# Kernel optimization log

Measured on AMD Instinct MI355X. Metric: run time of the kernel, lower is better.

## Reference

```python
import jax, jax.numpy as jnp
import numpy as np

B, N, DIM, H, DH = 8, 1024, 768, 12, 64  # batch, seq, d_model, heads, dim_head
INNER = H * DH


def setup_inputs() -> dict:
    key = jax.random.key(0)
    ks = jax.random.split(key, 6)
    s = 1.0 / np.sqrt(DIM)
    return {
        "x": jax.random.normal(ks[0], (B, N, DIM), dtype=jnp.float32),
        "Wq": jax.random.normal(ks[1], (DIM, INNER), dtype=jnp.float32) * s,
        "Wkv": jax.random.normal(ks[2], (DIM, 2 * INNER), dtype=jnp.float32) * s,
        "mix_pre": jax.random.normal(ks[3], (H, H), dtype=jnp.float32) * (1.0 / H),
        "mix_post": jax.random.normal(ks[4], (H, H), dtype=jnp.float32) * (1.0 / H),
        "Wo": jax.random.normal(ks[5], (INNER, DIM), dtype=jnp.float32) * s,
        "bo": jnp.zeros((DIM,), dtype=jnp.float32),
    }


def reference(x, Wq, Wkv, mix_pre, mix_post, Wo, bo):
    scale = DH ** -0.5
    q = x @ Wq                                   # [B,N,INNER]
    kv = x @ Wkv                                 # [B,N,2*INNER]
    k, v = jnp.split(kv, 2, axis=-1)
    split_heads = lambda t: t.reshape(B, N, H, DH).transpose(0, 2, 1, 3)  # [B,H,N,DH]
    q, k, v = split_heads(q), split_heads(k), split_heads(v)
    dots = jnp.einsum('bhid,bhjd->bhij', q, k) * scale
    dots = jnp.einsum('bhij,hg->bgij', dots, mix_pre)      # talking-heads pre-softmax
    attn = jax.nn.softmax(dots, axis=-1)
    attn = jnp.einsum('bhij,hg->bgij', attn, mix_post)     # talking-heads post-softmax
    o = jnp.einsum('bhij,bhjd->bhid', attn, v)             # [B,H,N,DH]
    o = o.transpose(0, 2, 1, 3).reshape(B, N, INNER)
    return o @ Wo + bo
```

## Files before the change

### kernel.cpp

```cpp
#include <hip/hip_runtime.h>
#include <cstdint>
#include <cstddef>

typedef unsigned short u16;
typedef unsigned int u32;

typedef __bf16 bf16x8 __attribute__((ext_vector_type(8)));
typedef float f32x4 __attribute__((ext_vector_type(4)));
typedef u32 u32x4 __attribute__((ext_vector_type(4)));
typedef u32 u32x2 __attribute__((ext_vector_type(2)));

#if defined(__has_builtin)
#if __has_builtin(__builtin_amdgcn_global_load_lds)
#define USE_GLL 1
#endif
#endif

typedef const __attribute__((address_space(1))) u32 gas_u32;
typedef __attribute__((address_space(3))) u32 las_u32;

__device__ inline float bf2f(u16 u) {
    union { u32 i; float f; } c; c.i = ((u32)u) << 16; return c.f;
}
__device__ inline u16 f2bf(float f) {
    union { float f; u32 i; } c; c.f = f;
    u32 u = c.i;
    return (u16)((u + 0x7fffu + ((u >> 16) & 1u)) >> 16);
}
__device__ inline f32x4 mfma16(u32x4 a, u32x4 b, f32x4 c) {
    return __builtin_amdgcn_mfma_f32_16x16x32_bf16(
        __builtin_bit_cast(bf16x8, a), __builtin_bit_cast(bf16x8, b), c, 0, 0, 0);
}
__device__ inline u32x4 cvt8(const float* p) {
    f32x4 a = *(const f32x4*)p, b = *(const f32x4*)(p + 4);
    u32x4 v;
    v[0] = (u32)f2bf(a[0]) | ((u32)f2bf(a[1]) << 16);
    v[1] = (u32)f2bf(a[2]) | ((u32)f2bf(a[3]) << 16);
    v[2] = (u32)f2bf(b[0]) | ((u32)f2bf(b[1]) << 16);
    v[3] = (u32)f2bf(b[2]) | ((u32)f2bf(b[3]) << 16);
    return v;
}

__device__ inline void bar_lds() {
    asm volatile("s_waitcnt lgkmcnt(0)" ::: "memory");
    __builtin_amdgcn_s_barrier();
    __builtin_amdgcn_sched_barrier(0);
}

__global__ __launch_bounds__(64) void k_detect(const u16* __restrict__ x, u32* __restrict__ flag)
{
    const int lane = threadIdx.x;
    int cnt = 0;
#pragma unroll
    for (int i = 0; i < 4; i++) {
        u32 e = (x[lane * 4 + i] >> 7) & 0xFF;
        cnt += (e >= 115 && e <= 133) ? 1 : 0;
    }
#pragma unroll
    for (int off = 1; off < 64; off <<= 1) cnt += __shfl_xor(cnt, off);
    if (lane == 0) *flag = (cnt >= 192) ? 1u : 0u;
}

__global__ __launch_bounds__(256) void k_convert_x(
    const void* __restrict__ X, u16* __restrict__ xb, const u32* __restrict__ flag)
{
    const bool isb = (*flag != 0);
    const size_t i = ((size_t)blockIdx.x * 256 + threadIdx.x) * 8;
    if (isb) *(u32x4*)(xb + i) = *(const u32x4*)((const u16*)X + i);
    else     *(u32x4*)(xb + i) = cvt8((const float*)X + i);
}

__global__ __launch_bounds__(256) void k_transpose_w(
    const void* __restrict__ Wq, const void* __restrict__ Wkv, const void* __restrict__ Wo,
    u16* __restrict__ WT, u16* __restrict__ WoT, const u32* __restrict__ flag)
{
    const bool isb = (*flag != 0);
    __shared__ __align__(16) u16 t[64][72];
    const int z = blockIdx.z;
    const void* src; u16* dst; int C;
    if (z == 0)      { src = Wq;  dst = WT;             C = 768;  }
    else if (z == 1) { src = Wkv; dst = WT + 768 * 768; C = 1536; }
    else             { src = Wo;  dst = WoT;            C = 768;  }
    const int c0 = blockIdx.y * 64;
    if (c0 >= C) return;
    const int k0 = blockIdx.x * 64;
    const int tid = threadIdx.x;
    const int r = tid >> 3, cc = (tid & 7) * 8;
    if (isb) {
        const u16* s = (const u16*)src;
        for (int rr = r; rr < 64; rr += 32)
            *(u32x4*)&t[rr][cc] = *(const u32x4*)(s + (size_t)(k0 + rr) * C + c0 + cc);
    } else {
        const float* s = (const float*)src;
        for (int rr = r; rr < 64; rr += 32)
            *(u32x4*)&t[rr][cc] = cvt8(s + (size_t)(k0 + rr) * C + c0 + cc);
    }
    __syncthreads();
    const int kk = (tid & 7) * 8;
    for (int ccc = tid >> 3; ccc < 64; ccc += 32) {
        __align__(16) u16 tmp[8];
#pragma unroll
        for (int s = 0; s < 8; s++) tmp[s] = t[kk + s][ccc];
        *(u32x4*)(dst + (size_t)(c0 + ccc) * 768 + k0 + kk) = *(u32x4*)tmp;
    }
}

__global__ __launch_bounds__(256) void k_transpose_v(
    const u16* __restrict__ v, u16* __restrict__ vt)
{
    __shared__ __align__(16) u16 t[64][72];
    const int bh = blockIdx.z;
    const int t0 = blockIdx.x * 64;
    const int tid = threadIdx.x;
    const int r = tid >> 3, cc = (tid & 7) * 8;
    for (int rr = r; rr < 64; rr += 32)
        *(u32x4*)&t[rr][cc] = *(const u32x4*)(v + ((size_t)bh * 1024 + t0 + rr) * 64 + cc);
    __syncthreads();
    const int kk = (tid & 7) * 8;
    for (int ccc = tid >> 3; ccc < 64; ccc += 32) {
        __align__(16) u16 tmp[8];
#pragma unroll
        for (int s = 0; s < 8; s++) tmp[s] = t[kk + s][ccc];
        *(u32x4*)(vt + ((size_t)bh * 64 + ccc) * 1024 + t0 + kk) = *(u32x4*)tmp;
    }
}

__device__ inline void stage_tile(const u16* __restrict__ gA, const u16* __restrict__ gB,
                                  u16* As, u16* Bs, int w, int lane)
{
    const int sr = lane >> 2, sc = (lane & 3) * 8;
#pragma unroll
    for (int i = 0; i < 2; i++) {
        const int rA = w * 16 + i * 64;
        const u16* ga = gA + (size_t)(rA + sr) * 768 + sc;
        const u16* gb = gB + (size_t)(rA + sr) * 768 + sc;
#ifdef USE_GLL
        __builtin_amdgcn_global_load_lds((gas_u32*)ga, (las_u32*)&As[rA * 32], 16, 0, 0);
        __builtin_amdgcn_global_load_lds((gas_u32*)gb, (las_u32*)&Bs[rA * 32], 16, 0, 0);
#else
        *(u32x4*)&As[(rA + sr) * 32 + sc] = *(const u32x4*)ga;
        *(u32x4*)&Bs[(rA + sr) * 32 + sc] = *(const u32x4*)gb;
#endif
    }
}

__global__ __launch_bounds__(256) void k_gemm_qkv(
    const u16* __restrict__ Xb, const u16* __restrict__ WT,
    u16* __restrict__ qb, u16* __restrict__ kb, u16* __restrict__ vb)
{
    __shared__ __align__(16) u16 As[128 * 32];
    __shared__ __align__(16) u16 Bs[128 * 32];
    const int tid = threadIdx.x;
    const int w = tid >> 6, lane = tid & 63, quad = lane >> 4, l15 = lane & 15;
    const int wr = w >> 1, wc = w & 1;
    const int m0 = blockIdx.y * 128, c0 = blockIdx.x * 128;
    f32x4 acc[4][4];
#pragma unroll
    for (int i = 0; i < 4; i++)
#pragma unroll
        for (int j = 0; j < 4; j++) acc[i][j] = (f32x4){0.f, 0.f, 0.f, 0.f};

    for (int k0 = 0; k0 < 768; k0 += 32) {
        __syncthreads();
        stage_tile(Xb + (size_t)m0 * 768 + k0, WT + (size_t)c0 * 768 + k0, As, Bs, w, lane);
        __syncthreads();
        u32x4 af[4], bfv[4];
#pragma unroll
        for (int mi = 0; mi < 4; mi++)
            af[mi] = *(const u32x4*)&As[(wr * 64 + mi * 16 + l15) * 32 + quad * 8];
#pragma unroll
        for (int ni = 0; ni < 4; ni++)
            bfv[ni] = *(const u32x4*)&Bs[(wc * 64 + ni * 16 + l15) * 32 + quad * 8];
#pragma unroll
        for (int mi = 0; mi < 4; mi++)
#pragma unroll
            for (int ni = 0; ni < 4; ni++)
                acc[mi][ni] = mfma16(af[mi], bfv[ni], acc[mi][ni]);
    }
#pragma unroll
    for (int mi = 0; mi < 4; mi++)
#pragma unroll
        for (int ni = 0; ni < 4; ni++) {
            const int c = c0 + wc * 64 + ni * 16 + l15;
            const int sector = c / 768, hc = c % 768;
            const int h = hc >> 6, d = hc & 63;
            u16* dst = sector == 0 ? qb : (sector == 1 ? kb : vb);
#pragma unroll
            for (int r = 0; r < 4; r++) {
                const int tok = m0 + wr * 64 + mi * 16 + quad * 4 + r;
                const int b = tok >> 10, n = tok & 1023;
                dst[(((size_t)b * 12 + h) * 1024 + n) * 64 + d] = f2bf(acc[mi][ni][r]);
            }
        }
}

__global__ __launch_bounds__(256) void k_gemm_out(
    const u16* __restrict__ O, const u16* __restrict__ WoT, const void* __restrict__ bo,
    float* __restrict__ out, const u32* __restrict__ flag)
{
    const bool isb = (*flag != 0);
    __shared__ __align__(16) u16 As[128 * 32];
    __shared__ __align__(16) u16 Bs[128 * 32];
    const int tid = threadIdx.x;
    const int w = tid >> 6, lane = tid & 63, quad = lane >> 4, l15 = lane & 15;
    const int wr = w >> 1, wc = w & 1;
    const int m0 = blockIdx.y * 128, c0 = blockIdx.x * 128;
    f32x4 acc[4][4];
#pragma unroll
    for (int i = 0; i < 4; i++)
#pragma unroll
        for (int j = 0; j < 4; j++) acc[i][j] = (f32x4){0.f, 0.f, 0.f, 0.f};

    for (int k0 = 0; k0 < 768; k0 += 32) {
        __syncthreads();
        stage_tile(O + (size_t)m0 * 768 + k0, WoT + (size_t)c0 * 768 + k0, As, Bs, w, lane);
        __syncthreads();
        u32x4 af[4], bfv[4];
#pragma unroll
        for (int mi = 0; mi < 4; mi++)
            af[mi] = *(const u32x4*)&As[(wr * 64 + mi * 16 + l15) * 32 + quad * 8];
#pragma unroll
        for (int ni = 0; ni < 4; ni++)
            bfv[ni] = *(const u32x4*)&Bs[(wc * 64 + ni * 16 + l15) * 32 + quad * 8];
#pragma unroll
        for (int mi = 0; mi < 4; mi++)
#pragma unroll
            for (int ni = 0; ni < 4; ni++)
                acc[mi][ni] = mfma16(af[mi], bfv[ni], acc[mi][ni]);
    }
#pragma unroll
    for (int mi = 0; mi < 4; mi++)
#pragma unroll
        for (int ni = 0; ni < 4; ni++) {
            const int c = c0 + wc * 64 + ni * 16 + l15;
            const float biasv = isb ? bf2f(((const u16*)bo)[c]) : ((const float*)bo)[c];
#pragma unroll
            for (int r = 0; r < 4; r++) {
                const int tok = m0 + wr * 64 + mi * 16 + quad * 4 + r;
                out[(size_t)tok * 768 + c] = acc[mi][ni][r] + biasv;
            }
        }
}

__device__ inline void stage_e(const u16* __restrict__ src, u16* dst, int w, int lane)
{
#pragma unroll
    for (int c = 0; c < 2; c++) {
        const int off = ((w * 2 + c) * 64 + lane) * 8;
#ifdef USE_GLL
        __builtin_amdgcn_global_load_lds((gas_u32*)(src + off), (las_u32*)(dst + off), 16, 0, 0);
#else
        *(u32x4*)(dst + off) = *(const u32x4*)(src + off);
#endif
    }
}

__global__ __launch_bounds__(768) void k_attn(
    const u16* __restrict__ qb, const u16* __restrict__ kb, const u16* __restrict__ vt,
    const void* __restrict__ mixpre, const void* __restrict__ mixpost,
    u16* __restrict__ ob, u16* __restrict__ E, const u32* __restrict__ flag, int tiles)
{
    __shared__ __align__(16) u16 LDSU[18432];
    __shared__ float invlT[256];
    __shared__ __align__(16) u16 Eslab[2][12296];
    u16* SP   = LDSU;
    u32* SP32 = (u32*)LDSU;
    u16* Abuf = LDSU;
    float* red = (float*)LDSU;

    const bool isb = (*flag != 0);
    const int tid = threadIdx.x;
    const int w = tid >> 6, lane = tid & 63, quad = lane >> 4, l15 = lane & 15;
    const int bid = blockIdx.x;
    const int b = bid & 7;
    const int nq = gridDim.x >> 3;
    u16* Ewg = E + (size_t)bid * (16384 * 12);

    u32x4 apre = (u32x4){0, 0, 0, 0};
    float mpostF[8];
#pragma unroll
    for (int j = 0; j < 8; j++) {
        const int h = quad * 8 + j;
        mpostF[j] = 0.f;
        if (quad < 2 && l15 < 12 && h < 12) {
            mpostF[j] = isb ? bf2f(((const u16*)mixpost)[h * 12 + l15])
                            : ((const float*)mixpost)[h * 12 + l15];
            u16 v1 = isb ? ((const u16*)mixpre)[h * 12 + l15]
                         : f2bf(((const float*)mixpre)[h * 12 + l15]);
            apre[j >> 1] |= ((u32)v1) << ((j & 1) * 16);
        }
    }

    const u16* kh = kb + ((size_t)b * 12 + w) * 1024 * 64;
    const u16* vh = vt + ((size_t)b * 12 + w) * 64 * 1024;

    for (int tt = 0; tt < tiles; tt++) {
        const int qx = (bid >> 3) + tt * nq;
        const int i0 = qx * 16;

        for (int n = tid; n < 1024; n += 768) { SP32[n * 9 + 6] = 0; SP32[n * 9 + 7] = 0; }

        const u16* qh = qb + (((size_t)b * 12 + w) * 1024 + i0) * 64;
        u32x4 aq[2];
#pragma unroll
        for (int kc = 0; kc < 2; kc++)
            aq[kc] = *(const u32x4*)(qh + l15 * 64 + kc * 32 + quad * 8);

        f32x4 part[6];
#pragma unroll
        for (int t = 0; t < 6; t++) part[t] = (f32x4){0.f, 0.f, 0.f, 0.f};

        for (int jt = 0; jt < 16; jt++) {
            const int j0 = jt * 64;
            f32x4 sc[4];
#pragma unroll
            for (int nt = 0; nt < 4; nt++) {
                f32x4 a = (f32x4){0.f, 0.f, 0.f, 0.f};
#pragma unroll
                for (int kc = 0; kc < 2; kc++) {
                    u32x4 bfr = *(const u32x4*)(kh + (size_t)(j0 + nt * 16 + l15) * 64 + kc * 32 + quad * 8);
                    a = mfma16(aq[kc], bfr, a);
                }
                sc[nt] = a;
            }
            bar_lds();
#pragma unroll
            for (int nt = 0; nt < 4; nt++)
#pragma unroll
                for (int r = 0; r < 4; r++)
                    SP[((quad * 4 + r) * 64 + nt * 16 + l15) * 18 + w] = f2bf(sc[nt][r] * 0.125f);
            bar_lds();
#pragma unroll
            for (int t = 0; t < 6; t++) {
                const int s = w + 12 * t;
                if (s < 64) {
                    const int row = s * 16 + l15;
                    u32x4 bfr = (u32x4){0, 0, 0, 0};
                    if (quad < 2) {
                        const u32* p = SP32 + row * 9 + quad * 4;
                        bfr[0] = p[0]; bfr[1] = p[1]; bfr[2] = p[2]; bfr[3] = p[3];
                    }
                    f32x4 d = mfma16(apre, bfr, (f32x4){0.f, 0.f, 0.f, 0.f});
                    const float e0 = __expf(d[0]), e1 = __expf(d[1]);
                    const float e2 = __expf(d[2]), e3 = __expf(d[3]);
                    part[t][0] += e0; part[t][1] += e1;
                    part[t][2] += e2; part[t][3] += e3;
                    if (quad < 3) {
                        u32x2 pk;
                        pk[0] = (u32)f2bf(e0) | ((u32)f2bf(e1) << 16);
                        pk[1] = (u32)f2bf(e2) | ((u32)f2bf(e3) << 16);
                        *(u32x2*)(Ewg + ((size_t)jt * 1024 + row) * 12 + quad * 4) = pk;
                    }
                }
            }
        }
        __syncthreads();
#pragma unroll
        for (int t = 0; t < 6; t++) {
            const int s = w + 12 * t;
            if (s < 64) {
#pragma unroll
                for (int r = 0; r < 4; r++) {
                    float v = part[t][r];
#pragma unroll
                    for (int off = 1; off < 16; off <<= 1) v += __shfl_xor(v, off);
                    if (l15 == 0) red[(((s >> 2) * 16) + quad * 4 + r) * 4 + (s & 3)] = v;
                }
            }
        }
        __syncthreads();
        if (tid < 256) {
            const int h = tid & 15;
            float v = 0.f;
            if (h < 12) {
                const float* q = &red[tid * 4];
                v = 1.f / (q[0] + q[1] + q[2] + q[3]);
            }
            invlT[tid] = v;
        }
        __syncthreads();

        stage_e(Ewg, Eslab[0], w, lane);

        u32x4 Afr[6];
#pragma unroll
        for (int t = 0; t < 6; t++) {
            const int s = w + 12 * t;
            Afr[t] = (u32x4){0, 0, 0, 0};
            if (s < 64 && quad < 2) {
                const int i = s >> 2;
#pragma unroll
                for (int j = 0; j < 8; j++) {
                    const u16 v = f2bf(mpostF[j] * invlT[i * 16 + quad * 8 + j]);
                    Afr[t][j >> 1] |= ((u32)v) << ((j & 1) * 16);
                }
            }
        }
        __syncthreads();

        f32x4 oacc[4];
#pragma unroll
        for (int nt = 0; nt < 4; nt++) oacc[nt] = (f32x4){0.f, 0.f, 0.f, 0.f};

        for (int jt = 0; jt < 16; jt++) {
            const int cur = jt & 1;
            const int j0 = jt * 64;
            if (jt < 15) {
                stage_e(Ewg + (size_t)(jt + 1) * 12288, Eslab[cur ^ 1], w, lane);
                asm volatile("s_waitcnt vmcnt(2)" ::: "memory");
            } else {
                asm volatile("s_waitcnt vmcnt(0)" ::: "memory");
            }
            __builtin_amdgcn_sched_barrier(0);
#pragma unroll
            for (int t = 0; t < 6; t++) {
                const int s = w + 12 * t;
                if (s < 64) {
                    const int row = s * 16 + l15, i = s >> 2, jq = s & 3;
                    u32x4 ef = (u32x4){0, 0, 0, 0};
                    if (quad < 2) {
                        const u16* ep = &Eslab[cur][row * 12 + quad * 8];
                        u32x2 lo = *(const u32x2*)ep;
                        u32x2 hi = *(const u32x2*)(ep + 4);
                        ef[0] = lo[0]; ef[1] = lo[1]; ef[2] = hi[0]; ef[3] = hi[1];
                    }
                    f32x4 am = mfma16(Afr[t], ef, (f32x4){0.f, 0.f, 0.f, 0.f});
#pragma unroll
                    for (int r = 0; r < 4; r++) {
                        const int g2 = quad * 4 + r;
                        if (g2 < 12)
                            Abuf[g2 * 1160 + i * 72 + jq * 16 + l15] = f2bf(am[r]);
                    }
                }
            }
            bar_lds();
#pragma unroll
            for (int kc = 0; kc < 2; kc++) {
                u32x4 af = *(const u32x4*)&Abuf[w * 1160 + l15 * 72 + kc * 32 + quad * 8];
#pragma unroll
                for (int nt = 0; nt < 4; nt++) {
                    u32x4 vf = *(const u32x4*)(vh + (size_t)(nt * 16 + l15) * 1024 + j0 + kc * 32 + quad * 8);
                    oacc[nt] = mfma16(af, vf, oacc[nt]);
                }
            }
            bar_lds();
        }
#pragma unroll
        for (int nt = 0; nt < 4; nt++)
#pragma unroll
            for (int r = 0; r < 4; r++)
                ob[((size_t)b * 1024 + i0 + quad * 4 + r) * 768 + w * 64 + nt * 16 + l15] =
                    f2bf(oacc[nt][r]);
    }
}

extern "C" void kernel_launch(void* const* d_in, const int* in_sizes, int n_in,
                              void* d_out, int out_size, void* d_ws, size_t ws_size,
                              hipStream_t stream)
{
    float* out = (float*)d_out;

    u32* flag = (u32*)d_ws;
    u16* WoT  = (u16*)d_ws + 128;
    u16* qb   = WoT + 768 * 768;
    u16* kb   = qb  + 6291456;
    u16* vtb  = kb  + 6291456;
    u16* obuf = vtb + 6291456;
    u16* vb   = obuf;
    u16* ez   = obuf + 6291456;
    u16* WT   = ez;
    u16* xb   = ez + 2304 * 768;
    u16* E    = ez;

    const size_t base   = 256 + 2ull * (768 * 768 + 4ull * 6291456);
    const size_t eslot  = 16384ull * 12 * 2;
    const size_t need1  = base + 512ull * eslot + 64;
    const size_t need2  = base + 256ull * eslot + 64;

    k_detect     <<<dim3(1), 64,  0, stream>>>((const u16*)d_in[0], flag);
    k_transpose_w<<<dim3(12, 24, 3), 256, 0, stream>>>(d_in[1], d_in[2], d_in[5], WT, WoT, flag);
    k_convert_x  <<<dim3(3072),      256, 0, stream>>>(d_in[0], xb, flag);
    k_gemm_qkv   <<<dim3(18, 64),    256, 0, stream>>>(xb, WT, qb, kb, vb);
    k_transpose_v<<<dim3(16, 1, 96), 256, 0, stream>>>(vb, vtb);
    if (ws_size >= need1)
        k_attn   <<<dim3(512), 768, 0, stream>>>(qb, kb, vtb, d_in[3], d_in[4], obuf, E, flag, 1);
    else
        k_attn   <<<dim3(256), 768, 0, stream>>>(qb, kb, vtb, d_in[3], d_in[4], obuf, E, flag, 2);
    k_gemm_out   <<<dim3(6, 64),     256, 0, stream>>>(obuf, WoT, d_in[6], out, flag);
}
```

Measured before the change: 447.8 us.

## Remap attention kernel to 16 waves with double-buffered score LDS

The talking-heads attention kernel moves from 12 waves (one per head) to 16 waves, where each wave handles one 16-column slice across three heads. It double-buffers the score and A-matrix LDS staging so one barrier per key tile can be dropped. It also rearranges the E scratch layout for contiguous 8-byte stores and reads, and uses the packed v_cvt_pk_bf16_f32 conversion. The goal is to balance the 64 mixing slices evenly across waves (the old mapping left idle slots) and to cut synchronisation. The costs are a larger LDS footprint and more register pressure at 1024 threads.

```diff
diff --git a/kernel.cpp b/kernel.cpp
--- a/kernel.cpp
+++ b/kernel.cpp
@@ -26,6 +26,9 @@
     union { float f; u32 i; } c; c.f = f;
     u32 u = c.i;
     return (u16)((u + 0x7fffu + ((u >> 16) & 1u)) >> 16);
+}
+__device__ inline u32 cvtpk(float lo, float hi) {
+    u32 r; asm("v_cvt_pk_bf16_f32 %0, %1, %2" : "=v"(r) : "v"(lo), "v"(hi)); return r;
 }
 __device__ inline f32x4 mfma16(u32x4 a, u32x4 b, f32x4 c) {
     return __builtin_amdgcn_mfma_f32_16x16x32_bf16(
@@ -244,33 +247,36 @@
 
 __device__ inline void stage_e(const u16* __restrict__ src, u16* dst, int w, int lane)
 {
-#pragma unroll
-    for (int c = 0; c < 2; c++) {
-        const int off = ((w * 2 + c) * 64 + lane) * 8;
+    const int o1 = (w * 64 + lane) * 8;
 #ifdef USE_GLL
-        __builtin_amdgcn_global_load_lds((gas_u32*)(src + off), (las_u32*)(dst + off), 16, 0, 0);
+    __builtin_amdgcn_global_load_lds((gas_u32*)(src + o1), (las_u32*)(dst + o1), 16, 0, 0);
 #else
-        *(u32x4*)(dst + off) = *(const u32x4*)(src + off);
+    *(u32x4*)(dst + o1) = *(const u32x4*)(src + o1);
 #endif
-    }
-}
-
-__global__ __launch_bounds__(768) void k_attn(
+    if (w < 8) {
+        const int o2 = ((16 + w) * 64 + lane) * 8;
+#ifdef USE_GLL
+        __builtin_amdgcn_global_load_lds((gas_u32*)(src + o2), (las_u32*)(dst + o2), 16, 0, 0);
+#else
+        *(u32x4*)(dst + o2) = *(const u32x4*)(src + o2);
+#endif
+    }
+}
+
+__global__ __launch_bounds__(1024) void k_attn(
     const u16* __restrict__ qb, const u16* __restrict__ kb, const u16* __restrict__ vt,
     const void* __restrict__ mixpre, const void* __restrict__ mixpost,
     u16* __restrict__ ob, u16* __restrict__ E, const u32* __restrict__ flag, int tiles)
 {
-    __shared__ __align__(16) u16 LDSU[18432];
+    __shared__ __align__(16) u16 SPd[2][1024 * 18];
     __shared__ float invlT[256];
-    __shared__ __align__(16) u16 Eslab[2][12296];
-    u16* SP   = LDSU;
-    u32* SP32 = (u32*)LDSU;
-    u16* Abuf = LDSU;
-    float* red = (float*)LDSU;
+    __shared__ __align__(16) u16 Eslab[2][12288];
+    float* red = (float*)&Eslab[0][0];
 
     const bool isb = (*flag != 0);
     const int tid = threadIdx.x;
     const int w = tid >> 6, lane = tid & 63, quad = lane >> 4, l15 = lane & 15;
+    const int nt = w & 3, h0 = w >> 2;
     const int bid = blockIdx.x;
     const int b = bid & 7;
     const int nq = gridDim.x >> 3;
@@ -291,84 +297,84 @@
         }
     }
 
-    const u16* kh = kb + ((size_t)b * 12 + w) * 1024 * 64;
-    const u16* vh = vt + ((size_t)b * 12 + w) * 64 * 1024;
-
     for (int tt = 0; tt < tiles; tt++) {
         const int qx = (bid >> 3) + tt * nq;
         const int i0 = qx * 16;
 
-        for (int n = tid; n < 1024; n += 768) { SP32[n * 9 + 6] = 0; SP32[n * 9 + 7] = 0; }
-
-        const u16* qh = qb + (((size_t)b * 12 + w) * 1024 + i0) * 64;
-        u32x4 aq[2];
-#pragma unroll
-        for (int kc = 0; kc < 2; kc++)
-            aq[kc] = *(const u32x4*)(qh + l15 * 64 + kc * 32 + quad * 8);
-
-        f32x4 part[6];
-#pragma unroll
-        for (int t = 0; t < 6; t++) part[t] = (f32x4){0.f, 0.f, 0.f, 0.f};
+        bar_lds();
+        {
+            u32* spz = (u32*)&SPd[0][0];
+            for (int n = tid; n < 2048; n += 1024) { spz[n * 9 + 6] = 0; spz[n * 9 + 7] = 0; }
+        }
+
+        u32x4 aq[3][2];
+#pragma unroll
+        for (int t = 0; t < 3; t++) {
+            const u16* qh = qb + (((size_t)b * 12 + (h0 + 4 * t)) * 1024 + i0) * 64;
+#pragma unroll
+            for (int kc = 0; kc < 2; kc++)
+                aq[t][kc] = *(const u32x4*)(qh + l15 * 64 + kc * 32 + quad * 8);
+        }
+
+        f32x4 part[4];
+#pragma unroll
+        for (int t = 0; t < 4; t++) part[t] = (f32x4){0.f, 0.f, 0.f, 0.f};
 
         for (int jt = 0; jt < 16; jt++) {
+            u16* SPc = &SPd[0][0] + (jt & 1) * (1024 * 18);
+            u32* SPc32 = (u32*)SPc;
             const int j0 = jt * 64;
-            f32x4 sc[4];
-#pragma unroll
-            for (int nt = 0; nt < 4; nt++) {
+#pragma unroll
+            for (int t = 0; t < 3; t++) {
+                const int h = h0 + 4 * t;
+                const u16* khp = kb + ((size_t)b * 12 + h) * 65536;
                 f32x4 a = (f32x4){0.f, 0.f, 0.f, 0.f};
 #pragma unroll
                 for (int kc = 0; kc < 2; kc++) {
-                    u32x4 bfr = *(const u32x4*)(kh + (size_t)(j0 + nt * 16 + l15) * 64 + kc * 32 + quad * 8);
-                    a = mfma16(aq[kc], bfr, a);
-                }
-                sc[nt] = a;
+                    u32x4 bfr = *(const u32x4*)(khp + (size_t)(j0 + nt * 16 + l15) * 64 + kc * 32 + quad * 8);
+                    a = mfma16(aq[t][kc], bfr, a);
+                }
+#pragma unroll
+                for (int r = 0; r < 4; r++)
+                    SPc[((quad * 4 + r) * 64 + nt * 16 + l15) * 18 + h] = f2bf(a[r] * 0.125f);
             }
             bar_lds();
 #pragma unroll
-            for (int nt = 0; nt < 4; nt++)
-#pragma unroll
-                for (int r = 0; r < 4; r++)
-                    SP[((quad * 4 + r) * 64 + nt * 16 + l15) * 18 + w] = f2bf(sc[nt][r] * 0.125f);
-            bar_lds();
-#pragma unroll
-            for (int t = 0; t < 6; t++) {
-                const int s = w + 12 * t;
-                if (s < 64) {
-                    const int row = s * 16 + l15;
-                    u32x4 bfr = (u32x4){0, 0, 0, 0};
-                    if (quad < 2) {
-                        const u32* p = SP32 + row * 9 + quad * 4;
-                        bfr[0] = p[0]; bfr[1] = p[1]; bfr[2] = p[2]; bfr[3] = p[3];
-                    }
-                    f32x4 d = mfma16(apre, bfr, (f32x4){0.f, 0.f, 0.f, 0.f});
-                    const float e0 = __expf(d[0]), e1 = __expf(d[1]);
-                    const float e2 = __expf(d[2]), e3 = __expf(d[3]);
-                    part[t][0] += e0; part[t][1] += e1;
-                    part[t][2] += e2; part[t][3] += e3;
-                    if (quad < 3) {
-                        u32x2 pk;
-                        pk[0] = (u32)f2bf(e0) | ((u32)f2bf(e1) << 16);
-                        pk[1] = (u32)f2bf(e2) | ((u32)f2bf(e3) << 16);
-                        *(u32x2*)(Ewg + ((size_t)jt * 1024 + row) * 12 + quad * 4) = pk;
-                    }
+            for (int t = 0; t < 4; t++) {
+                const int s = w + 16 * t;
+                const int row = s * 16 + l15;
+                u32x4 bfr = (u32x4){0, 0, 0, 0};
+                if (quad < 2) {
+                    const u32* p = SPc32 + row * 9 + quad * 4;
+                    bfr[0] = p[0]; bfr[1] = p[1]; bfr[2] = p[2]; bfr[3] = p[3];
+                }
+                f32x4 d = mfma16(apre, bfr, (f32x4){0.f, 0.f, 0.f, 0.f});
+                const float e0 = __expf(d[0]), e1 = __expf(d[1]);
+                const float e2 = __expf(d[2]), e3 = __expf(d[3]);
+                part[t][0] += e0; part[t][1] += e1;
+                part[t][2] += e2; part[t][3] += e3;
+                if (quad < 3) {
+                    u32x2 pk;
+                    pk[0] = cvtpk(e0, e1);
+                    pk[1] = cvtpk(e2, e3);
+                    *(u32x2*)(Ewg + ((size_t)(jt * 64 + s) * 3 + quad) * 64 + l15 * 4) = pk;
                 }
             }
         }
         __syncthreads();
-#pragma unroll
-        for (int t = 0; t < 6; t++) {
-            const int s = w + 12 * t;
-            if (s < 64) {
-#pragma unroll
-                for (int r = 0; r < 4; r++) {
-                    float v = part[t][r];
-#pragma unroll
-                    for (int off = 1; off < 16; off <<= 1) v += __shfl_xor(v, off);
-                    if (l15 == 0) red[(((s >> 2) * 16) + quad * 4 + r) * 4 + (s & 3)] = v;
-                }
-            }
-        }
-        __syncthreads();
+
+#pragma unroll
+        for (int t = 0; t < 4; t++) {
+            const int s = w + 16 * t;
+#pragma unroll
+            for (int r = 0; r < 4; r++) {
+                float v = part[t][r];
+#pragma unroll
+                for (int off = 1; off < 16; off <<= 1) v += __shfl_xor(v, off);
+                if (l15 == 0) red[(((s >> 2) * 16) + quad * 4 + r) * 4 + (s & 3)] = v;
+            }
+        }
+        bar_lds();
         if (tid < 256) {
             const int h = tid & 15;
             float v = 0.f;
@@ -378,79 +384,83 @@
             }
             invlT[tid] = v;
         }
+        bar_lds();
+
+        u32x4 Afr[4];
+#pragma unroll
+        for (int t = 0; t < 4; t++) {
+            const int s = w + 16 * t;
+            const int i = s >> 2;
+            Afr[t] = (u32x4){0, 0, 0, 0};
+            if (quad < 2) {
+#pragma unroll
+                for (int j = 0; j < 8; j++) {
+                    const int h = quad * 8 + j;
+                    if (h < 12) {
+                        const u16 v = f2bf(mpostF[j] * invlT[i * 16 + h]);
+                        Afr[t][j >> 1] |= ((u32)v) << ((j & 1) * 16);
+                    }
+                }
+            }
+        }
+        stage_e(Ewg, Eslab[0], w, lane);
         __syncthreads();
 
-        stage_e(Ewg, Eslab[0], w, lane);
-
-        u32x4 Afr[6];
-#pragma unroll
-        for (int t = 0; t < 6; t++) {
-            const int s = w + 12 * t;
-            Afr[t] = (u32x4){0, 0, 0, 0};
-            if (s < 64 && quad < 2) {
-                const int i = s >> 2;
-#pragma unroll
-                for (int j = 0; j < 8; j++) {
-                    const u16 v = f2bf(mpostF[j] * invlT[i * 16 + quad * 8 + j]);
-                    Afr[t][j >> 1] |= ((u32)v) << ((j & 1) * 16);
-                }
-            }
-        }
-        __syncthreads();
-
-        f32x4 oacc[4];
-#pragma unroll
-        for (int nt = 0; nt < 4; nt++) oacc[nt] = (f32x4){0.f, 0.f, 0.f, 0.f};
+        f32x4 oacc[3];
+#pragma unroll
+        for (int t = 0; t < 3; t++) oacc[t] = (f32x4){0.f, 0.f, 0.f, 0.f};
 
         for (int jt = 0; jt < 16; jt++) {
             const int cur = jt & 1;
+            u16* Ab = &SPd[0][0] + cur * 13920;
             const int j0 = jt * 64;
-            if (jt < 15) {
+            if (jt < 15)
                 stage_e(Ewg + (size_t)(jt + 1) * 12288, Eslab[cur ^ 1], w, lane);
-                asm volatile("s_waitcnt vmcnt(2)" ::: "memory");
-            } else {
-                asm volatile("s_waitcnt vmcnt(0)" ::: "memory");
-            }
-            __builtin_amdgcn_sched_barrier(0);
-#pragma unroll
-            for (int t = 0; t < 6; t++) {
-                const int s = w + 12 * t;
-                if (s < 64) {
-                    const int row = s * 16 + l15, i = s >> 2, jq = s & 3;
-                    u32x4 ef = (u32x4){0, 0, 0, 0};
-                    if (quad < 2) {
-                        const u16* ep = &Eslab[cur][row * 12 + quad * 8];
-                        u32x2 lo = *(const u32x2*)ep;
-                        u32x2 hi = *(const u32x2*)(ep + 4);
-                        ef[0] = lo[0]; ef[1] = lo[1]; ef[2] = hi[0]; ef[3] = hi[1];
+#pragma unroll
+            for (int t = 0; t < 4; t++) {
+                const int s = w + 16 * t;
+                const int i = s >> 2, jq = s & 3;
+                u32x4 ef = (u32x4){0, 0, 0, 0};
+                if (quad < 2) {
+                    const u32* sl = (const u32*)&Eslab[cur][0];
+                    const int base = (s * 3 + quad * 2) * 32 + l15 * 2;
+                    u32x2 lo = *(const u32x2*)(sl + base);
+                    ef[0] = lo[0]; ef[1] = lo[1];
+                    if (quad == 0) {
+                        u32x2 hi = *(const u32x2*)(sl + base + 32);
+                        ef[2] = hi[0]; ef[3] = hi[1];
                     }
-                    f32x4 am = mfma16(Afr[t], ef, (f32x4){0.f, 0.f, 0.f, 0.f});
-#pragma unroll
-                    for (int r = 0; r < 4; r++) {
-                        const int g2 = quad * 4 + r;
-                        if (g2 < 12)
-                            Abuf[g2 * 1160 + i * 72 + jq * 16 + l15] = f2bf(am[r]);
-                    }
-                }
-            }
+                }
+                f32x4 am = mfma16(Afr[t], ef, (f32x4){0.f, 0.f, 0.f, 0.f});
+#pragma unroll
+                for (int r = 0; r < 4; r++) {
+                    const int g2 = quad * 4 + r;
+                    if (g2 < 12)
+                        Ab[g2 * 1160 + i * 72 + jq * 16 + l15] = f2bf(am[r]);
+                }
+            }
+            asm volatile("s_waitcnt vmcnt(0)" ::: "memory");
             bar_lds();
 #pragma unroll
-            for (int kc = 0; kc < 2; kc++) {
-                u32x4 af = *(const u32x4*)&Abuf[w * 1160 + l15 * 72 + kc * 32 + quad * 8];
-#pragma unroll
-                for (int nt = 0; nt < 4; nt++) {
-                    u32x4 vf = *(const u32x4*)(vh + (size_t)(nt * 16 + l15) * 1024 + j0 + kc * 32 + quad * 8);
-                    oacc[nt] = mfma16(af, vf, oacc[nt]);
-                }
-            }
-            bar_lds();
-        }
-#pragma unroll
-        for (int nt = 0; nt < 4; nt++)
+            for (int t = 0; t < 3; t++) {
+                const int h = h0 + 4 * t;
+                const u16* vhp = vt + ((size_t)b * 12 + h) * 65536;
+#pragma unroll
+                for (int kc = 0; kc < 2; kc++) {
+                    u32x4 af = *(const u32x4*)&Ab[h * 1160 + l15 * 72 + kc * 32 + quad * 8];
+                    u32x4 vf = *(const u32x4*)(vhp + (size_t)(nt * 16 + l15) * 1024 + j0 + kc * 32 + quad * 8);
+                    oacc[t] = mfma16(af, vf, oacc[t]);
+                }
+            }
+        }
+#pragma unroll
+        for (int t = 0; t < 3; t++) {
+            const int h = h0 + 4 * t;
 #pragma unroll
             for (int r = 0; r < 4; r++)
-                ob[((size_t)b * 1024 + i0 + quad * 4 + r) * 768 + w * 64 + nt * 16 + l15] =
-                    f2bf(oacc[nt][r]);
+                ob[((size_t)b * 1024 + i0 + quad * 4 + r) * 768 + h * 64 + nt * 16 + l15] =
+                    f2bf(oacc[t][r]);
+        }
     }
 }
 
@@ -483,8 +493,8 @@
     k_gemm_qkv   <<<dim3(18, 64),    256, 0, stream>>>(xb, WT, qb, kb, vb);
     k_transpose_v<<<dim3(16, 1, 96), 256, 0, stream>>>(vb, vtb);
     if (ws_size >= need1)
-        k_attn   <<<dim3(512), 768, 0, stream>>>(qb, kb, vtb, d_in[3], d_in[4], obuf, E, flag, 1);
+        k_attn   <<<dim3(512), 1024, 0, stream>>>(qb, kb, vtb, d_in[3], d_in[4], obuf, E, flag, 1);
     else
-        k_attn   <<<dim3(256), 768, 0, stream>>>(qb, kb, vtb, d_in[3], d_in[4], obuf, E, flag, 2);
+        k_attn   <<<dim3(256), 1024, 0, stream>>>(qb, kb, vtb, d_in[3], d_in[4], obuf, E, flag, 2);
     k_gemm_out   <<<dim3(6, 64),     256, 0, stream>>>(obuf, WoT, d_in[6], out, flag);
 }
```

After: 472.6 us. 1.06x slower.

## Double-buffer score and mixed-attention LDS tiles to halve barriers per step

Applied to the files above, without the earlier changes.

Both inner loops now use two LDS buffers. The QK^T scores for tile jt+1 are written while tile jt is mixed and exponentiated, and the post-mix attention tile jt+1 is produced while tile jt is multiplied by V. This removes one block barrier per iteration and lets the MFMA work of adjacent tiles overlap. The f32-to-bf16 packing of the exponentials switches to the hardware v_cvt_pk_bf16_f32 instruction. The cost is doubled LDS usage, which may lower occupancy, and more complex buffer indexing.

```diff
diff --git a/kernel.cpp b/kernel.cpp
--- a/kernel.cpp
+++ b/kernel.cpp
@@ -26,6 +26,9 @@
     union { float f; u32 i; } c; c.f = f;
     u32 u = c.i;
     return (u16)((u + 0x7fffu + ((u >> 16) & 1u)) >> 16);
+}
+__device__ inline u32 cvtpk(float lo, float hi) {
+    u32 r; asm("v_cvt_pk_bf16_f32 %0, %1, %2" : "=v"(r) : "v"(lo), "v"(hi)); return r;
 }
 __device__ inline f32x4 mfma16(u32x4 a, u32x4 b, f32x4 c) {
     return __builtin_amdgcn_mfma_f32_16x16x32_bf16(
@@ -260,13 +263,10 @@
     const void* __restrict__ mixpre, const void* __restrict__ mixpost,
     u16* __restrict__ ob, u16* __restrict__ E, const u32* __restrict__ flag, int tiles)
 {
-    __shared__ __align__(16) u16 LDSU[18432];
+    __shared__ __align__(16) u16 SPd[2][18432];
     __shared__ float invlT[256];
     __shared__ __align__(16) u16 Eslab[2][12296];
-    u16* SP   = LDSU;
-    u32* SP32 = (u32*)LDSU;
-    u16* Abuf = LDSU;
-    float* red = (float*)LDSU;
+    float* red = (float*)&SPd[0][0];
 
     const bool isb = (*flag != 0);
     const int tid = threadIdx.x;
@@ -291,14 +291,17 @@
         }
     }
 
-    const u16* kh = kb + ((size_t)b * 12 + w) * 1024 * 64;
-    const u16* vh = vt + ((size_t)b * 12 + w) * 64 * 1024;
+    const u16* kh = kb + ((size_t)b * 12 + w) * 65536;
+    const u16* vh = vt + ((size_t)b * 12 + w) * 65536;
 
     for (int tt = 0; tt < tiles; tt++) {
         const int qx = (bid >> 3) + tt * nq;
         const int i0 = qx * 16;
 
-        for (int n = tid; n < 1024; n += 768) { SP32[n * 9 + 6] = 0; SP32[n * 9 + 7] = 0; }
+        {
+            u32* spz = (u32*)&SPd[0][0];
+            for (int n = tid; n < 2048; n += 768) { spz[n * 9 + 6] = 0; spz[n * 9 + 7] = 0; }
+        }
 
         const u16* qh = qb + (((size_t)b * 12 + w) * 1024 + i0) * 64;
         u32x4 aq[2];
@@ -310,26 +313,41 @@
 #pragma unroll
         for (int t = 0; t < 6; t++) part[t] = (f32x4){0.f, 0.f, 0.f, 0.f};
 
-        for (int jt = 0; jt < 16; jt++) {
-            const int j0 = jt * 64;
-            f32x4 sc[4];
+        {
+            u16* SPc = &SPd[0][0];
 #pragma unroll
             for (int nt = 0; nt < 4; nt++) {
                 f32x4 a = (f32x4){0.f, 0.f, 0.f, 0.f};
 #pragma unroll
                 for (int kc = 0; kc < 2; kc++) {
-                    u32x4 bfr = *(const u32x4*)(kh + (size_t)(j0 + nt * 16 + l15) * 64 + kc * 32 + quad * 8);
+                    u32x4 bfr = *(const u32x4*)(kh + (size_t)(nt * 16 + l15) * 64 + kc * 32 + quad * 8);
                     a = mfma16(aq[kc], bfr, a);
                 }
-                sc[nt] = a;
-            }
-            bar_lds();
-#pragma unroll
-            for (int nt = 0; nt < 4; nt++)
 #pragma unroll
                 for (int r = 0; r < 4; r++)
-                    SP[((quad * 4 + r) * 64 + nt * 16 + l15) * 18 + w] = f2bf(sc[nt][r] * 0.125f);
-            bar_lds();
+                    SPc[((quad * 4 + r) * 64 + nt * 16 + l15) * 18 + w] = f2bf(a[r] * 0.125f);
+            }
+        }
+        bar_lds();
+
+        for (int jt = 0; jt < 16; jt++) {
+            if (jt < 15) {
+                u16* SPn = &SPd[0][0] + ((jt + 1) & 1) * 18432;
+                const int j0n = (jt + 1) * 64;
+#pragma unroll
+                for (int nt = 0; nt < 4; nt++) {
+                    f32x4 a = (f32x4){0.f, 0.f, 0.f, 0.f};
+#pragma unroll
+                    for (int kc = 0; kc < 2; kc++) {
+                        u32x4 bfr = *(const u32x4*)(kh + (size_t)(j0n + nt * 16 + l15) * 64 + kc * 32 + quad * 8);
+                        a = mfma16(aq[kc], bfr, a);
+                    }
+#pragma unroll
+                    for (int r = 0; r < 4; r++)
+                        SPn[((quad * 4 + r) * 64 + nt * 16 + l15) * 18 + w] = f2bf(a[r] * 0.125f);
+                }
+            }
+            const u32* SPc32 = (const u32*)(&SPd[0][0] + (jt & 1) * 18432);
 #pragma unroll
             for (int t = 0; t < 6; t++) {
                 const int s = w + 12 * t;
@@ -337,7 +355,7 @@
                     const int row = s * 16 + l15;
                     u32x4 bfr = (u32x4){0, 0, 0, 0};
                     if (quad < 2) {
-                        const u32* p = SP32 + row * 9 + quad * 4;
+                        const u32* p = SPc32 + row * 9 + quad * 4;
                         bfr[0] = p[0]; bfr[1] = p[1]; bfr[2] = p[2]; bfr[3] = p[3];
                     }
                     f32x4 d = mfma16(apre, bfr, (f32x4){0.f, 0.f, 0.f, 0.f});
@@ -347,14 +365,16 @@
                     part[t][2] += e2; part[t][3] += e3;
                     if (quad < 3) {
                         u32x2 pk;
-                        pk[0] = (u32)f2bf(e0) | ((u32)f2bf(e1) << 16);
-                        pk[1] = (u32)f2bf(e2) | ((u32)f2bf(e3) << 16);
+                        pk[0] = cvtpk(e0, e1);
+                        pk[1] = cvtpk(e2, e3);
                         *(u32x2*)(Ewg + ((size_t)jt * 1024 + row) * 12 + quad * 4) = pk;
                     }
                 }
             }
+            bar_lds();
         }
         __syncthreads();
+
 #pragma unroll
         for (int t = 0; t < 6; t++) {
             const int s = w + 12 * t;
@@ -368,7 +388,7 @@
                 }
             }
         }
-        __syncthreads();
+        bar_lds();
         if (tid < 256) {
             const int h = tid & 15;
             float v = 0.f;
@@ -378,9 +398,7 @@
             }
             invlT[tid] = v;
         }
-        __syncthreads();
-
-        stage_e(Ewg, Eslab[0], w, lane);
+        bar_lds();
 
         u32x4 Afr[6];
 #pragma unroll
@@ -396,22 +414,14 @@
                 }
             }
         }
-        __syncthreads();
-
-        f32x4 oacc[4];
-#pragma unroll
-        for (int nt = 0; nt < 4; nt++) oacc[nt] = (f32x4){0.f, 0.f, 0.f, 0.f};
-
-        for (int jt = 0; jt < 16; jt++) {
-            const int cur = jt & 1;
-            const int j0 = jt * 64;
-            if (jt < 15) {
-                stage_e(Ewg + (size_t)(jt + 1) * 12288, Eslab[cur ^ 1], w, lane);
-                asm volatile("s_waitcnt vmcnt(2)" ::: "memory");
-            } else {
-                asm volatile("s_waitcnt vmcnt(0)" ::: "memory");
-            }
-            __builtin_amdgcn_sched_barrier(0);
+        stage_e(Ewg, &Eslab[0][0], w, lane);
+        stage_e(Ewg + 12288, &Eslab[1][0], w, lane);
+        asm volatile("s_waitcnt vmcnt(0)" ::: "memory");
+        __builtin_amdgcn_sched_barrier(0);
+        bar_lds();
+
+        {
+            u16* Ab = &SPd[0][0];
 #pragma unroll
             for (int t = 0; t < 6; t++) {
                 const int s = w + 12 * t;
@@ -419,7 +429,7 @@
                     const int row = s * 16 + l15, i = s >> 2, jq = s & 3;
                     u32x4 ef = (u32x4){0, 0, 0, 0};
                     if (quad < 2) {
-                        const u16* ep = &Eslab[cur][row * 12 + quad * 8];
+                        const u16* ep = &Eslab[0][row * 12 + quad * 8];
                         u32x2 lo = *(const u32x2*)ep;
                         u32x2 hi = *(const u32x2*)(ep + 4);
                         ef[0] = lo[0]; ef[1] = lo[1]; ef[2] = hi[0]; ef[3] = hi[1];
@@ -429,18 +439,58 @@
                     for (int r = 0; r < 4; r++) {
                         const int g2 = quad * 4 + r;
                         if (g2 < 12)
-                            Abuf[g2 * 1160 + i * 72 + jq * 16 + l15] = f2bf(am[r]);
-                    }
-                }
-            }
-            bar_lds();
-#pragma unroll
-            for (int kc = 0; kc < 2; kc++) {
-                u32x4 af = *(const u32x4*)&Abuf[w * 1160 + l15 * 72 + kc * 32 + quad * 8];
-#pragma unroll
-                for (int nt = 0; nt < 4; nt++) {
-                    u32x4 vf = *(const u32x4*)(vh + (size_t)(nt * 16 + l15) * 1024 + j0 + kc * 32 + quad * 8);
-                    oacc[nt] = mfma16(af, vf, oacc[nt]);
+                            Ab[g2 * 1160 + i * 72 + jq * 16 + l15] = f2bf(am[r]);
+                    }
+                }
+            }
+        }
+        bar_lds();
+
+        f32x4 oacc[4];
+#pragma unroll
+        for (int nt = 0; nt < 4; nt++) oacc[nt] = (f32x4){0.f, 0.f, 0.f, 0.f};
+
+        for (int jt = 0; jt < 16; jt++) {
+            asm volatile("s_waitcnt vmcnt(0)" ::: "memory");
+            __builtin_amdgcn_sched_barrier(0);
+            if (jt < 14)
+                stage_e(Ewg + (size_t)(jt + 2) * 12288, &Eslab[jt & 1][0], w, lane);
+            if (jt < 15) {
+                const int nb = (jt + 1) & 1;
+                u16* Ab = &SPd[0][0] + nb * 18432;
+#pragma unroll
+                for (int t = 0; t < 6; t++) {
+                    const int s = w + 12 * t;
+                    if (s < 64) {
+                        const int row = s * 16 + l15, i = s >> 2, jq = s & 3;
+                        u32x4 ef = (u32x4){0, 0, 0, 0};
+                        if (quad < 2) {
+                            const u16* ep = &Eslab[nb][row * 12 + quad * 8];
+                            u32x2 lo = *(const u32x2*)ep;
+                            u32x2 hi = *(const u32x2*)(ep + 4);
+                            ef[0] = lo[0]; ef[1] = lo[1]; ef[2] = hi[0]; ef[3] = hi[1];
+                        }
+                        f32x4 am = mfma16(Afr[t], ef, (f32x4){0.f, 0.f, 0.f, 0.f});
+#pragma unroll
+                        for (int r = 0; r < 4; r++) {
+                            const int g2 = quad * 4 + r;
+                            if (g2 < 12)
+                                Ab[g2 * 1160 + i * 72 + jq * 16 + l15] = f2bf(am[r]);
+                        }
+                    }
+                }
+            }
+            {
+                const u16* Ab = &SPd[0][0] + (jt & 1) * 18432;
+                const int j0 = jt * 64;
+#pragma unroll
+                for (int kc = 0; kc < 2; kc++) {
+                    u32x4 af = *(const u32x4*)&Ab[w * 1160 + l15 * 72 + kc * 32 + quad * 8];
+#pragma unroll
+                    for (int nt = 0; nt < 4; nt++) {
+                        u32x4 vf = *(const u32x4*)(vh + (size_t)(nt * 16 + l15) * 1024 + j0 + kc * 32 + quad * 8);
+                        oacc[nt] = mfma16(af, vf, oacc[nt]);
+                    }
                 }
             }
             bar_lds();
```

Result: slower. 470.3 us (+5.0%).

## Recompute attention scores in second pass instead of spilling exp tiles to global

Applied to the files above, without the earlier changes.

The attention kernel no longer writes the bf16 exp(scores) slabs to a global scratch buffer and streams them back through double-buffered LDS. The first pass now only accumulates softmax row sums, and the second pass recomputes QK^T, the pre-mix and exp per key tile, storing the result directly into LDS. This removes a large global write/read round trip and the workspace-size dependent launch, at the cost of doing the score GEMM and exponentials twice. It also uses a packed bf16 conversion instruction and gives the score, A and E buffers separate LDS regions.

```diff
diff --git a/kernel.cpp b/kernel.cpp
--- a/kernel.cpp
+++ b/kernel.cpp
@@ -26,6 +26,9 @@
     union { float f; u32 i; } c; c.f = f;
     u32 u = c.i;
     return (u16)((u + 0x7fffu + ((u >> 16) & 1u)) >> 16);
+}
+__device__ inline u32 cvtpk(float lo, float hi) {
+    u32 r; asm("v_cvt_pk_bf16_f32 %0, %1, %2" : "=v"(r) : "v"(lo), "v"(hi)); return r;
 }
 __device__ inline f32x4 mfma16(u32x4 a, u32x4 b, f32x4 c) {
     return __builtin_amdgcn_mfma_f32_16x16x32_bf16(
@@ -242,39 +245,24 @@
         }
 }
 
-__device__ inline void stage_e(const u16* __restrict__ src, u16* dst, int w, int lane)
-{
-#pragma unroll
-    for (int c = 0; c < 2; c++) {
-        const int off = ((w * 2 + c) * 64 + lane) * 8;
-#ifdef USE_GLL
-        __builtin_amdgcn_global_load_lds((gas_u32*)(src + off), (las_u32*)(dst + off), 16, 0, 0);
-#else
-        *(u32x4*)(dst + off) = *(const u32x4*)(src + off);
-#endif
-    }
-}
-
 __global__ __launch_bounds__(768) void k_attn(
     const u16* __restrict__ qb, const u16* __restrict__ kb, const u16* __restrict__ vt,
     const void* __restrict__ mixpre, const void* __restrict__ mixpost,
-    u16* __restrict__ ob, u16* __restrict__ E, const u32* __restrict__ flag, int tiles)
-{
-    __shared__ __align__(16) u16 LDSU[18432];
+    u16* __restrict__ ob, const u32* __restrict__ flag)
+{
+    __shared__ __align__(16) u16 SP[18432];
+    __shared__ __align__(16) u16 Abuf[13920];
+    __shared__ __align__(16) u16 Elds[12296];
     __shared__ float invlT[256];
-    __shared__ __align__(16) u16 Eslab[2][12296];
-    u16* SP   = LDSU;
-    u32* SP32 = (u32*)LDSU;
-    u16* Abuf = LDSU;
-    float* red = (float*)LDSU;
+    u32* SP32 = (u32*)SP;
+    float* red = (float*)&Elds[0];
 
     const bool isb = (*flag != 0);
     const int tid = threadIdx.x;
     const int w = tid >> 6, lane = tid & 63, quad = lane >> 4, l15 = lane & 15;
     const int bid = blockIdx.x;
     const int b = bid & 7;
-    const int nq = gridDim.x >> 3;
-    u16* Ewg = E + (size_t)bid * (16384 * 12);
+    const int i0 = (bid >> 3) * 16;
 
     u32x4 apre = (u32x4){0, 0, 0, 0};
     float mpostF[8];
@@ -291,167 +279,190 @@
         }
     }
 
-    const u16* kh = kb + ((size_t)b * 12 + w) * 1024 * 64;
-    const u16* vh = vt + ((size_t)b * 12 + w) * 64 * 1024;
-
-    for (int tt = 0; tt < tiles; tt++) {
-        const int qx = (bid >> 3) + tt * nq;
-        const int i0 = qx * 16;
-
+    const u16* kh = kb + ((size_t)b * 12 + w) * 65536;
+    const u16* vh = vt + ((size_t)b * 12 + w) * 65536;
+
+    {
         for (int n = tid; n < 1024; n += 768) { SP32[n * 9 + 6] = 0; SP32[n * 9 + 7] = 0; }
-
-        const u16* qh = qb + (((size_t)b * 12 + w) * 1024 + i0) * 64;
-        u32x4 aq[2];
-#pragma unroll
-        for (int kc = 0; kc < 2; kc++)
-            aq[kc] = *(const u32x4*)(qh + l15 * 64 + kc * 32 + quad * 8);
-
-        f32x4 part[6];
-#pragma unroll
-        for (int t = 0; t < 6; t++) part[t] = (f32x4){0.f, 0.f, 0.f, 0.f};
-
-        for (int jt = 0; jt < 16; jt++) {
-            const int j0 = jt * 64;
-            f32x4 sc[4];
-#pragma unroll
-            for (int nt = 0; nt < 4; nt++) {
-                f32x4 a = (f32x4){0.f, 0.f, 0.f, 0.f};
-#pragma unroll
-                for (int kc = 0; kc < 2; kc++) {
-                    u32x4 bfr = *(const u32x4*)(kh + (size_t)(j0 + nt * 16 + l15) * 64 + kc * 32 + quad * 8);
-                    a = mfma16(aq[kc], bfr, a);
-                }
-                sc[nt] = a;
-            }
-            bar_lds();
-#pragma unroll
-            for (int nt = 0; nt < 4; nt++)
-#pragma unroll
-                for (int r = 0; r < 4; r++)
-                    SP[((quad * 4 + r) * 64 + nt * 16 + l15) * 18 + w] = f2bf(sc[nt][r] * 0.125f);
-            bar_lds();
-#pragma unroll
-            for (int t = 0; t < 6; t++) {
-                const int s = w + 12 * t;
-                if (s < 64) {
-                    const int row = s * 16 + l15;
-                    u32x4 bfr = (u32x4){0, 0, 0, 0};
-                    if (quad < 2) {
-                        const u32* p = SP32 + row * 9 + quad * 4;
-                        bfr[0] = p[0]; bfr[1] = p[1]; bfr[2] = p[2]; bfr[3] = p[3];
-                    }
-                    f32x4 d = mfma16(apre, bfr, (f32x4){0.f, 0.f, 0.f, 0.f});
-                    const float e0 = __expf(d[0]), e1 = __expf(d[1]);
-                    const float e2 = __expf(d[2]), e3 = __expf(d[3]);
-                    part[t][0] += e0; part[t][1] += e1;
-                    part[t][2] += e2; part[t][3] += e3;
-                    if (quad < 3) {
-                        u32x2 pk;
-                        pk[0] = (u32)f2bf(e0) | ((u32)f2bf(e1) << 16);
-                        pk[1] = (u32)f2bf(e2) | ((u32)f2bf(e3) << 16);
-                        *(u32x2*)(Ewg + ((size_t)jt * 1024 + row) * 12 + quad * 4) = pk;
-                    }
-                }
-            }
-        }
-        __syncthreads();
+    }
+
+    const u16* qh = qb + (((size_t)b * 12 + w) * 1024 + i0) * 64;
+    u32x4 aq[2];
+#pragma unroll
+    for (int kc = 0; kc < 2; kc++)
+        aq[kc] = *(const u32x4*)(qh + l15 * 64 + kc * 32 + quad * 8);
+
+    f32x4 part[6];
+#pragma unroll
+    for (int t = 0; t < 6; t++) part[t] = (f32x4){0.f, 0.f, 0.f, 0.f};
+
+    for (int jt = 0; jt < 16; jt++) {
+        const int j0 = jt * 64;
+        f32x4 sc[4];
+#pragma unroll
+        for (int nt = 0; nt < 4; nt++) {
+            f32x4 a = (f32x4){0.f, 0.f, 0.f, 0.f};
+#pragma unroll
+            for (int kc = 0; kc < 2; kc++) {
+                u32x4 bfr = *(const u32x4*)(kh + (size_t)(j0 + nt * 16 + l15) * 64 + kc * 32 + quad * 8);
+                a = mfma16(aq[kc], bfr, a);
+            }
+            sc[nt] = a;
+        }
+        bar_lds();
+#pragma unroll
+        for (int nt = 0; nt < 4; nt++)
+#pragma unroll
+            for (int r = 0; r < 4; r++)
+                SP[((quad * 4 + r) * 64 + nt * 16 + l15) * 18 + w] = f2bf(sc[nt][r] * 0.125f);
+        bar_lds();
 #pragma unroll
         for (int t = 0; t < 6; t++) {
             const int s = w + 12 * t;
             if (s < 64) {
-#pragma unroll
-                for (int r = 0; r < 4; r++) {
-                    float v = part[t][r];
-#pragma unroll
-                    for (int off = 1; off < 16; off <<= 1) v += __shfl_xor(v, off);
-                    if (l15 == 0) red[(((s >> 2) * 16) + quad * 4 + r) * 4 + (s & 3)] = v;
+                const int row = s * 16 + l15;
+                u32x4 bfr = (u32x4){0, 0, 0, 0};
+                if (quad < 2) {
+                    const u32* p = SP32 + row * 9 + quad * 4;
+                    bfr[0] = p[0]; bfr[1] = p[1]; bfr[2] = p[2]; bfr[3] = p[3];
                 }
-            }
-        }
-        __syncthreads();
-        if (tid < 256) {
-            const int h = tid & 15;
-            float v = 0.f;
-            if (h < 12) {
-                const float* q = &red[tid * 4];
-                v = 1.f / (q[0] + q[1] + q[2] + q[3]);
-            }
-            invlT[tid] = v;
-        }
-        __syncthreads();
-
-        stage_e(Ewg, Eslab[0], w, lane);
-
-        u32x4 Afr[6];
+                f32x4 d = mfma16(apre, bfr, (f32x4){0.f, 0.f, 0.f, 0.f});
+                part[t][0] += __expf(d[0]); part[t][1] += __expf(d[1]);
+                part[t][2] += __expf(d[2]); part[t][3] += __expf(d[3]);
+            }
+        }
+    }
+
+#pragma unroll
+    for (int t = 0; t < 6; t++) {
+        const int s = w + 12 * t;
+        if (s < 64) {
+#pragma unroll
+            for (int r = 0; r < 4; r++) {
+                float v = part[t][r];
+#pragma unroll
+                for (int off = 1; off < 16; off <<= 1) v += __shfl_xor(v, off);
+                if (l15 == 0) red[(((s >> 2) * 16) + quad * 4 + r) * 4 + (s & 3)] = v;
+            }
+        }
+    }
+    bar_lds();
+    if (tid < 256) {
+        const int h = tid & 15;
+        float v = 0.f;
+        if (h < 12) {
+            const float* q = &red[tid * 4];
+            v = 1.f / (q[0] + q[1] + q[2] + q[3]);
+        }
+        invlT[tid] = v;
+    }
+    bar_lds();
+
+    {
+        u32* ez = (u32*)&Elds[0];
+        for (int n = tid; n < 6148; n += 768) ez[n] = 0;
+    }
+    u32x4 Afr[6];
+#pragma unroll
+    for (int t = 0; t < 6; t++) {
+        const int s = w + 12 * t;
+        Afr[t] = (u32x4){0, 0, 0, 0};
+        if (s < 64 && quad < 2) {
+            const int i = s >> 2;
+#pragma unroll
+            for (int j = 0; j < 8; j++) {
+                const u16 v = f2bf(mpostF[j] * invlT[i * 16 + quad * 8 + j]);
+                Afr[t][j >> 1] |= ((u32)v) << ((j & 1) * 16);
+            }
+        }
+    }
+    bar_lds();
+
+    f32x4 oacc[4];
+#pragma unroll
+    for (int nt = 0; nt < 4; nt++) oacc[nt] = (f32x4){0.f, 0.f, 0.f, 0.f};
+
+    for (int jt = 0; jt < 16; jt++) {
+        const int j0 = jt * 64;
+        f32x4 sc[4];
+#pragma unroll
+        for (int nt = 0; nt < 4; nt++) {
+            f32x4 a = (f32x4){0.f, 0.f, 0.f, 0.f};
+#pragma unroll
+            for (int kc = 0; kc < 2; kc++) {
+                u32x4 bfr = *(const u32x4*)(kh + (size_t)(j0 + nt * 16 + l15) * 64 + kc * 32 + quad * 8);
+                a = mfma16(aq[kc], bfr, a);
+            }
+            sc[nt] = a;
+        }
+        bar_lds();
+#pragma unroll
+        for (int nt = 0; nt < 4; nt++)
+#pragma unroll
+            for (int r = 0; r < 4; r++)
+                SP[((quad * 4 + r) * 64 + nt * 16 + l15) * 18 + w] = f2bf(sc[nt][r] * 0.125f);
+        bar_lds();
 #pragma unroll
         for (int t = 0; t < 6; t++) {
             const int s = w + 12 * t;
-            Afr[t] = (u32x4){0, 0, 0, 0};
-            if (s < 64 && quad < 2) {
-                const int i = s >> 2;
-#pragma unroll
-                for (int j = 0; j < 8; j++) {
-                    const u16 v = f2bf(mpostF[j] * invlT[i * 16 + quad * 8 + j]);
-                    Afr[t][j >> 1] |= ((u32)v) << ((j & 1) * 16);
+            if (s < 64) {
+                const int row = s * 16 + l15;
+                u32x4 bfr = (u32x4){0, 0, 0, 0};
+                if (quad < 2) {
+                    const u32* p = SP32 + row * 9 + quad * 4;
+                    bfr[0] = p[0]; bfr[1] = p[1]; bfr[2] = p[2]; bfr[3] = p[3];
                 }
-            }
-        }
-        __syncthreads();
-
-        f32x4 oacc[4];
-#pragma unroll
-        for (int nt = 0; nt < 4; nt++) oacc[nt] = (f32x4){0.f, 0.f, 0.f, 0.f};
-
-        for (int jt = 0; jt < 16; jt++) {
-            const int cur = jt & 1;
-            const int j0 = jt * 64;
-            if (jt < 15) {
-                stage_e(Ewg + (size_t)(jt + 1) * 12288, Eslab[cur ^ 1], w, lane);
-                asm volatile("s_waitcnt vmcnt(2)" ::: "memory");
-            } else {
-                asm volatile("s_waitcnt vmcnt(0)" ::: "memory");
-            }
-            __builtin_amdgcn_sched_barrier(0);
-#pragma unroll
-            for (int t = 0; t < 6; t++) {
-                const int s = w + 12 * t;
-                if (s < 64) {
-                    const int row = s * 16 + l15, i = s >> 2, jq = s & 3;
-                    u32x4 ef = (u32x4){0, 0, 0, 0};
-                    if (quad < 2) {
-                        const u16* ep = &Eslab[cur][row * 12 + quad * 8];
-                        u32x2 lo = *(const u32x2*)ep;
-                        u32x2 hi = *(const u32x2*)(ep + 4);
-                        ef[0] = lo[0]; ef[1] = lo[1]; ef[2] = hi[0]; ef[3] = hi[1];
-                    }
-                    f32x4 am = mfma16(Afr[t], ef, (f32x4){0.f, 0.f, 0.f, 0.f});
-#pragma unroll
-                    for (int r = 0; r < 4; r++) {
-                        const int g2 = quad * 4 + r;
-                        if (g2 < 12)
-                            Abuf[g2 * 1160 + i * 72 + jq * 16 + l15] = f2bf(am[r]);
-                    }
+                f32x4 d = mfma16(apre, bfr, (f32x4){0.f, 0.f, 0.f, 0.f});
+                const float e0 = __expf(d[0]), e1 = __expf(d[1]);
+                const float e2 = __expf(d[2]), e3 = __expf(d[3]);
+                if (quad < 3) {
+                    u32x2 pk;
+                    pk[0] = cvtpk(e0, e1);
+                    pk[1] = cvtpk(e2, e3);
+                    *(u32x2*)(&Elds[row * 12 + quad * 4]) = pk;
                 }
             }
-            bar_lds();
-#pragma unroll
-            for (int kc = 0; kc < 2; kc++) {
-                u32x4 af = *(const u32x4*)&Abuf[w * 1160 + l15 * 72 + kc * 32 + quad * 8];
-#pragma unroll
-                for (int nt = 0; nt < 4; nt++) {
-                    u32x4 vf = *(const u32x4*)(vh + (size_t)(nt * 16 + l15) * 1024 + j0 + kc * 32 + quad * 8);
-                    oacc[nt] = mfma16(af, vf, oacc[nt]);
+        }
+        asm volatile("s_waitcnt lgkmcnt(0)" ::: "memory");
+        __builtin_amdgcn_sched_barrier(0);
+#pragma unroll
+        for (int t = 0; t < 6; t++) {
+            const int s = w + 12 * t;
+            if (s < 64) {
+                const int row = s * 16 + l15, i = s >> 2, jq = s & 3;
+                u32x4 ef = (u32x4){0, 0, 0, 0};
+                if (quad < 2) {
+                    const u16* ep = &Elds[row * 12 + quad * 8];
+                    u32x2 lo = *(const u32x2*)ep;
+                    u32x2 hi = *(const u32x2*)(ep + 4);
+                    ef[0] = lo[0]; ef[1] = lo[1]; ef[2] = hi[0]; ef[3] = hi[1];
                 }
-            }
-            bar_lds();
-        }
-#pragma unroll
-        for (int nt = 0; nt < 4; nt++)
-#pragma unroll
-            for (int r = 0; r < 4; r++)
-                ob[((size_t)b * 1024 + i0 + quad * 4 + r) * 768 + w * 64 + nt * 16 + l15] =
-                    f2bf(oacc[nt][r]);
-    }
+                f32x4 am = mfma16(Afr[t], ef, (f32x4){0.f, 0.f, 0.f, 0.f});
+#pragma unroll
+                for (int r = 0; r < 4; r++) {
+                    const int g2 = quad * 4 + r;
+                    if (g2 < 12)
+                        Abuf[g2 * 1160 + i * 72 + jq * 16 + l15] = f2bf(am[r]);
+                }
+            }
+        }
+        bar_lds();
+#pragma unroll
+        for (int kc = 0; kc < 2; kc++) {
+            u32x4 af = *(const u32x4*)&Abuf[w * 1160 + l15 * 72 + kc * 32 + quad * 8];
+#pragma unroll
+            for (int nt = 0; nt < 4; nt++) {
+                u32x4 vf = *(const u32x4*)(vh + (size_t)(nt * 16 + l15) * 1024 + j0 + kc * 32 + quad * 8);
+                oacc[nt] = mfma16(af, vf, oacc[nt]);
+            }
+        }
+    }
+#pragma unroll
+    for (int nt = 0; nt < 4; nt++)
+#pragma unroll
+        for (int r = 0; r < 4; r++)
+            ob[((size_t)b * 1024 + i0 + quad * 4 + r) * 768 + w * 64 + nt * 16 + l15] =
+                f2bf(oacc[nt][r]);
 }
 
 extern "C" void kernel_launch(void* const* d_in, const int* in_sizes, int n_in,
@@ -470,21 +481,12 @@
     u16* ez   = obuf + 6291456;
     u16* WT   = ez;
     u16* xb   = ez + 2304 * 768;
-    u16* E    = ez;
-
-    const size_t base   = 256 + 2ull * (768 * 768 + 4ull * 6291456);
-    const size_t eslot  = 16384ull * 12 * 2;
-    const size_t need1  = base + 512ull * eslot + 64;
-    const size_t need2  = base + 256ull * eslot + 64;
 
     k_detect     <<<dim3(1), 64,  0, stream>>>((const u16*)d_in[0], flag);
     k_transpose_w<<<dim3(12, 24, 3), 256, 0, stream>>>(d_in[1], d_in[2], d_in[5], WT, WoT, flag);
     k_convert_x  <<<dim3(3072),      256, 0, stream>>>(d_in[0], xb, flag);
     k_gemm_qkv   <<<dim3(18, 64),    256, 0, stream>>>(xb, WT, qb, kb, vb);
     k_transpose_v<<<dim3(16, 1, 96), 256, 0, stream>>>(vb, vtb);
-    if (ws_size >= need1)
-        k_attn   <<<dim3(512), 768, 0, stream>>>(qb, kb, vtb, d_in[3], d_in[4], obuf, E, flag, 1);
-    else
-        k_attn   <<<dim3(256), 768, 0, stream>>>(qb, kb, vtb, d_in[3], d_in[4], obuf, E, flag, 2);
+    k_attn       <<<dim3(512), 768,  0, stream>>>(qb, kb, vtb, d_in[3], d_in[4], obuf, flag);
     k_gemm_out   <<<dim3(6, 64),     256, 0, stream>>>(obuf, WoT, d_in[6], out, flag);
 }
```

After: 539.0 us. 1.2x slower.
